# Kernel optimization log

Hardware: AMD Instinct MI355X
Metric: run time of the kernel (lower is better)

Reference implementation:

```python
import jax, jax.numpy as jnp
import numpy as np

B, T, C = 8, 2048, 1024


def setup_inputs() -> dict:
    key = jax.random.key(0)
    ks = jax.random.split(key, 7)
    s = 0.02  # typical init scale for weights
    return {
        "x": jax.random.normal(ks[0], (B, T, C), jnp.float32),
        "wq": jax.random.normal(ks[1], (C, C), jnp.float32) * s,
        "bq": jax.random.normal(ks[2], (C,), jnp.float32) * s,
        "wk": jax.random.normal(ks[3], (C, C), jnp.float32) * s,
        "bk": jax.random.normal(ks[4], (C,), jnp.float32) * s,
        "wv": jax.random.normal(ks[5], (C, C), jnp.float32) * s,
        "bv": jax.random.normal(ks[6], (C,), jnp.float32) * s,
    }


def reference(x, wq, bq, wk, bk, wv, bv):
    # x: [B, T, C]; torch Linear stores weight as [out, in] -> x @ W.T + b
    Bx, Tx, Cx = x.shape
    Q = x @ wq.T + bq  # [B, T, C]
    K = x @ wk.T + bk
    V = x @ wv.T + bv
    # NOTE: source computes K @ Q^T (keys index rows, queries index columns)
    scores = jnp.einsum("btc,bsc->bts", K, Q) / jnp.sqrt(jnp.float32(Cx))  # [B, T, T]
    causal = jnp.tril(jnp.ones((Tx, Tx), dtype=bool))  # mask==0 above diagonal
    scores = jnp.where(causal, scores, -jnp.inf)
    # torch masked_fill with a (1,1,T,T) mask broadcasts scores to (1,B,T,T)
    scores = scores[None]  # [1, B, T, T]
    w = jax.nn.softmax(scores, axis=-1)
    out = jnp.einsum("abts,bsc->abtc", w, V)  # [1, B, T, C]
    return out
```

## Files before the change

kernel.cpp:

```cpp
#include <hip/hip_runtime.h>
#include <stdint.h>

typedef unsigned short u16;
typedef __attribute__((ext_vector_type(8))) __bf16 bf16x8;
typedef __attribute__((ext_vector_type(4))) float f32x4;

#define DEVI __device__ __forceinline__

DEVI u16 f32_to_bf16(float f) {
  uint32_t u = __builtin_bit_cast(uint32_t, f);
  u += 0x7FFFu + ((u >> 16) & 1u);
  return (u16)(u >> 16);
}

DEVI void gl2lds16(const void* g, void* l) {
  __builtin_amdgcn_global_load_lds(
      (const __attribute__((address_space(1))) void*)g,
      (__attribute__((address_space(3))) void*)l, 16, 0, 0);
}

#define SMEM_U16 17408

#define S_BATCH 2228224

DEVI void gemm_bt_mainloop(const u16* __restrict__ A, const u16* __restrict__ B,
                           int lda, int ldb, int kIters,
                           u16* As, u16* Bs, f32x4 (&acc)[4][4]) {
  const int tid = threadIdx.x;
  const int lane = tid & 63;
  const int wid = tid >> 6;
  const int wr = wid >> 1, wc = wid & 1;
  const int l15 = lane & 15, quad = lane >> 4;

  const int srow = tid >> 3;
  const int sgrp = ((tid & 7) - srow) & 7;
  const u16* Ag = A + (size_t)srow * lda + sgrp * 8;
  const u16* Bg = B + (size_t)srow * ldb + sgrp * 8;
  char* AsDst = (char*)As + tid * 16;
  char* BsDst = (char*)Bs + tid * 16;

  const int a_row0 = wr * 64 + l15;
  const int b_row0 = wc * 64 + l15;

  for (int kb = 0; kb < kIters; ++kb) {
#pragma unroll
    for (int r = 0; r < 4; ++r) {
      gl2lds16(Ag + (size_t)(r * 32) * lda, AsDst + r * 4096);
      gl2lds16(Bg + (size_t)(r * 32) * ldb, BsDst + r * 4096);
    }
    Ag += 64;
    Bg += 64;
    __syncthreads();
#pragma unroll
    for (int kk = 0; kk < 2; ++kk) {
      const int gA = ((kk * 4 + quad + a_row0) & 7) * 8;
      const int gB = ((kk * 4 + quad + b_row0) & 7) * 8;
      bf16x8 af[4], bfr[4];
#pragma unroll
      for (int i = 0; i < 4; ++i)
        af[i] = *(const bf16x8*)(As + (a_row0 + i * 16) * 64 + gA);
#pragma unroll
      for (int j = 0; j < 4; ++j)
        bfr[j] = *(const bf16x8*)(Bs + (b_row0 + j * 16) * 64 + gB);
#pragma unroll
      for (int i = 0; i < 4; ++i)
#pragma unroll
        for (int j = 0; j < 4; ++j)
          acc[i][j] = __builtin_amdgcn_mfma_f32_16x16x32_bf16(af[i], bfr[j],
                                                              acc[i][j], 0, 0, 0);
    }
    __syncthreads();
  }
}

DEVI void store_tile_bf16(const u16* tile, u16* __restrict__ out, int ld_out) {
  const int tid = threadIdx.x;
  const int c0 = (tid & 15) * 8;
#pragma unroll
  for (int rr = 0; rr < 8; ++rr) {
    const int row = rr * 16 + (tid >> 4);
    const uint4 v = *(const uint4*)(tile + row * 136 + c0);
    *(uint4*)(out + (size_t)row * ld_out + c0) = v;
  }
}

__global__ void cast_f32_to_bf16_kernel(const float* __restrict__ src,
                                        u16* __restrict__ dst, int n4) {
  int i = blockIdx.x * blockDim.x + threadIdx.x;
  const int stride = gridDim.x * blockDim.x;
  for (; i < n4; i += stride) {
    const float4 v = ((const float4*)src)[i];
    ushort4 o;
    o.x = f32_to_bf16(v.x);
    o.y = f32_to_bf16(v.y);
    o.z = f32_to_bf16(v.z);
    o.w = f32_to_bf16(v.w);
    ((ushort4*)dst)[i] = o;
  }
}

__global__ void cast_w_kernel(const float* __restrict__ wq,
                              const float* __restrict__ wk,
                              const float* __restrict__ wv,
                              u16* __restrict__ wb, float* __restrict__ sums) {
  const int z = blockIdx.y;
  if (z == 3) {
    int i = blockIdx.x * blockDim.x + threadIdx.x;
    if (i < 4096) ((float4*)sums)[i] = (float4){0.f, 0.f, 0.f, 0.f};
    return;
  }
  const float* src = (z == 0) ? wq : (z == 1) ? wk : wv;
  u16* dst = wb + (size_t)z * 1048576;
  int i = blockIdx.x * blockDim.x + threadIdx.x;
  const int stride = gridDim.x * blockDim.x;
  for (; i < 262144; i += stride) {
    const float4 v = ((const float4*)src)[i];
    ushort4 o;
    o.x = f32_to_bf16(v.x);
    o.y = f32_to_bf16(v.y);
    o.z = f32_to_bf16(v.z);
    o.w = f32_to_bf16(v.w);
    ((ushort4*)dst)[i] = o;
  }
}

__global__ __launch_bounds__(256) void qkv_kernel(
    const u16* __restrict__ xb, const u16* __restrict__ wb,
    const float* __restrict__ bq, const float* __restrict__ bk,
    const float* __restrict__ bv, u16* __restrict__ Qb, u16* __restrict__ Kb,
    u16* __restrict__ Vt) {
  __shared__ __align__(16) u16 smem[SMEM_U16];
  u16* As = smem;
  u16* Bs = smem + 8192;

  const int id = blockIdx.x;
  const int xcd = id & 7;
  const int local = id >> 3;
  const int chunk = local >> 6;
  const int li = local & 63;
  const int x = (chunk % 3) * 8 + (li & 7);
  const int y = xcd * 16 + (chunk / 3) * 8 + (li >> 3);
  const int m0 = y * 128;
  const int z = x >> 3;
  const int n0 = (x & 7) * 128;
  const float* bias = (z == 0) ? bq : (z == 1) ? bk : bv;

  f32x4 acc[4][4];
#pragma unroll
  for (int i = 0; i < 4; ++i)
#pragma unroll
    for (int j = 0; j < 4; ++j) acc[i][j] = (f32x4){0.f, 0.f, 0.f, 0.f};

  const int tid = threadIdx.x;
  const int lane = tid & 63, wid = tid >> 6;
  const int wr = wid >> 1, wc = wid & 1;
  const int l15 = lane & 15, quad = lane >> 4;

  if (z < 2) {
    gemm_bt_mainloop(wb + (size_t)(x * 128) * 1024, xb + (size_t)m0 * 1024,
                     1024, 1024, 16, As, Bs, acc);
#pragma unroll
    for (int i = 0; i < 4; ++i) {
      const int c0 = wr * 64 + i * 16 + quad * 4;
      const float4 b4 = *(const float4*)(bias + n0 + c0);
#pragma unroll
      for (int j = 0; j < 4; ++j) {
        const int t = wc * 64 + j * 16 + l15;
        ushort4 o;
        o.x = f32_to_bf16(acc[i][j][0] + b4.x);
        o.y = f32_to_bf16(acc[i][j][1] + b4.y);
        o.z = f32_to_bf16(acc[i][j][2] + b4.z);
        o.w = f32_to_bf16(acc[i][j][3] + b4.w);
        *(ushort4*)(smem + t * 136 + c0) = o;
      }
    }
    __syncthreads();
    u16* Out = ((z == 0) ? Qb : Kb) + (size_t)m0 * 1024 + n0;
    store_tile_bf16(smem, Out, 1024);
  } else {
    gemm_bt_mainloop(xb + (size_t)m0 * 1024, wb + (size_t)(x * 128) * 1024,
                     1024, 1024, 16, As, Bs, acc);
#pragma unroll
    for (int j = 0; j < 4; ++j) {
      const int c = wc * 64 + j * 16 + l15;
      const float bb = bias[n0 + c];
#pragma unroll
      for (int i = 0; i < 4; ++i) {
        const int t = wr * 64 + i * 16 + quad * 4;
        ushort4 o;
        o.x = f32_to_bf16(acc[i][j][0] + bb);
        o.y = f32_to_bf16(acc[i][j][1] + bb);
        o.z = f32_to_bf16(acc[i][j][2] + bb);
        o.w = f32_to_bf16(acc[i][j][3] + bb);
        *(ushort4*)(smem + c * 136 + t) = o;
      }
    }
    __syncthreads();
    const int bidx = m0 >> 11;
    const int t0 = m0 & 2047;
    u16* Out = Vt + ((size_t)bidx * 1024 + n0) * 2048 + t0;
    store_tile_bf16(smem, Out, 2048);
  }
}

__global__ __launch_bounds__(256) void score_kernel(const u16* __restrict__ Kb,
                                                    const u16* __restrict__ Qb,
                                                    u16* __restrict__ Spk,
                                                    float* __restrict__ sums) {
  const int b = blockIdx.x & 7;
  const int l = 135 - (blockIdx.x >> 3);
  int rt = (int)((sqrtf(8.f * l + 1.f) - 1.f) * 0.5f);
  int ct = l - rt * (rt + 1) / 2;
  if (ct > rt) { ++rt; ct = l - rt * (rt + 1) / 2; }
  if (ct < 0)  { --rt; ct = l - rt * (rt + 1) / 2; }

  __shared__ __align__(16) u16 smem[SMEM_U16];
  u16* As = smem;
  u16* Bs = smem + 8192;

  f32x4 acc[4][4];
#pragma unroll
  for (int i = 0; i < 4; ++i)
#pragma unroll
    for (int j = 0; j < 4; ++j) acc[i][j] = (f32x4){0.f, 0.f, 0.f, 0.f};

  const u16* A = Qb + ((size_t)b * 2048 + ct * 128) * 1024;
  const u16* B = Kb + ((size_t)b * 2048 + rt * 128) * 1024;
  gemm_bt_mainloop(A, B, 1024, 1024, 16, As, Bs, acc);

  const int tid = threadIdx.x;
  const int lane = tid & 63, wid = tid >> 6;
  const int wr = wid >> 1, wc = wid & 1;
  const int l15 = lane & 15, quad = lane >> 4;
  const bool diag = (rt == ct);

  float sj[4] = {0.f, 0.f, 0.f, 0.f};
#pragma unroll
  for (int i = 0; i < 4; ++i) {
    const int s0 = wr * 64 + i * 16 + quad * 4;
#pragma unroll
    for (int j = 0; j < 4; ++j) {
      const int t = wc * 64 + j * 16 + l15;
      ushort4 o;
      float e[4];
#pragma unroll
      for (int r = 0; r < 4; ++r) {
        float v = __expf(acc[i][j][r] * 0.03125f);
        if (diag && (s0 + r) > t) v = 0.f;
        e[r] = v;
        sj[j] += v;
      }
      o.x = f32_to_bf16(e[0]);
      o.y = f32_to_bf16(e[1]);
      o.z = f32_to_bf16(e[2]);
      o.w = f32_to_bf16(e[3]);
      *(ushort4*)(smem + t * 136 + s0) = o;
    }
  }
#pragma unroll
  for (int j = 0; j < 4; ++j) {
    float v = sj[j];
    v += __shfl_xor(v, 16);
    v += __shfl_xor(v, 32);
    if (quad == 0)
      atomicAdd(&sums[(size_t)b * 2048 + rt * 128 + wc * 64 + j * 16 + l15], v);
  }
  __syncthreads();
  const int ld = (rt + 1) * 128;
  u16* Out = Spk + (size_t)b * S_BATCH + (size_t)(rt * (rt + 1) / 2) * 16384 +
             ct * 128;
  store_tile_bf16(smem, Out, ld);
}

__global__ __launch_bounds__(256) void pv_kernel(const u16* __restrict__ Spk,
                                                 const u16* __restrict__ Vt,
                                                 const float* __restrict__ sums,
                                                 float* __restrict__ Out) {
  const int b = blockIdx.x & 7;
  const int local = 127 - (blockIdx.x >> 3);
  const int rt = local >> 3;
  const int ct = local & 7;

  __shared__ __align__(16) u16 smem[SMEM_U16];
  u16* As = smem;
  u16* Bs = smem + 8192;
  float* ftile = (float*)smem;

  f32x4 acc[4][4];
#pragma unroll
  for (int i = 0; i < 4; ++i)
#pragma unroll
    for (int j = 0; j < 4; ++j) acc[i][j] = (f32x4){0.f, 0.f, 0.f, 0.f};

  const u16* A = Vt + ((size_t)b * 1024 + ct * 128) * 2048;
  const u16* B = Spk + (size_t)b * S_BATCH +
                 (size_t)(rt * (rt + 1) / 2) * 16384;
  const int ldb = (rt + 1) * 128;
  gemm_bt_mainloop(A, B, 2048, ldb, (rt + 1) * 2, As, Bs, acc);

  const int tid = threadIdx.x;
  const int lane = tid & 63, wid = tid >> 6;
  const int wr = wid >> 1, wc = wid & 1;
  const int l15 = lane & 15, quad = lane >> 4;

  const float* sumsb = sums + (size_t)b * 2048 + rt * 128;
  float* Ob = Out + (size_t)b * 2048 * 1024 + (size_t)(rt * 128) * 1024 +
              ct * 128;
#pragma unroll
  for (int h = 0; h < 2; ++h) {
    if (wc == h) {
#pragma unroll
      for (int j = 0; j < 4; ++j) {
        const int tl = j * 16 + l15;
        const float iv = 1.0f / sumsb[h * 64 + tl];
#pragma unroll
        for (int i = 0; i < 4; ++i) {
          const int c0 = wr * 64 + i * 16 + quad * 4;
          float4 v;
          v.x = acc[i][j][0] * iv;
          v.y = acc[i][j][1] * iv;
          v.z = acc[i][j][2] * iv;
          v.w = acc[i][j][3] * iv;
          *(float4*)(ftile + tl * 132 + c0) = v;
        }
      }
    }
    __syncthreads();
#pragma unroll
    for (int rr = 0; rr < 8; ++rr) {
      const int row = rr * 8 + (tid >> 5);
      const int c0 = (tid & 31) * 4;
      const float4 v = *(const float4*)(ftile + row * 132 + c0);
      *(float4*)(Ob + (size_t)(h * 64 + row) * 1024 + c0) = v;
    }
    __syncthreads();
  }
}

extern "C" void kernel_launch(void* const* d_in, const int* in_sizes, int n_in,
                              void* d_out, int out_size, void* d_ws,
                              size_t ws_size, hipStream_t stream) {
  const float* x = (const float*)d_in[0];
  const float* wq = (const float*)d_in[1];
  const float* bq = (const float*)d_in[2];
  const float* wk = (const float*)d_in[3];
  const float* bk = (const float*)d_in[4];
  const float* wv = (const float*)d_in[5];
  const float* bv = (const float*)d_in[6];
  float* out = (float*)d_out;
  char* ws = (char*)d_ws;

  u16* Qb = (u16*)(ws);
  u16* Kb = (u16*)(ws + ((size_t)32 << 20));
  u16* Vt = (u16*)(ws + ((size_t)64 << 20));
  u16* Spk = (u16*)(ws + ((size_t)96 << 20));
  u16* xb = (u16*)(ws + ((size_t)96 << 20));
  float* sums = (float*)(ws + ((size_t)132 << 20));
  u16* wb = (u16*)(ws + ((size_t)134 << 20));

  cast_f32_to_bf16_kernel<<<16384, 256, 0, stream>>>(x, xb, 16777216 / 4);
  cast_w_kernel<<<dim3(512, 4), 256, 0, stream>>>(wq, wk, wv, wb, sums);

  qkv_kernel<<<3072, 256, 0, stream>>>(xb, wb, bq, bk, bv, Qb, Kb, Vt);

  score_kernel<<<8 * 136, 256, 0, stream>>>(Kb, Qb, Spk, sums);

  pv_kernel<<<8 * 128, 256, 0, stream>>>(Spk, Vt, sums, out);
}
```

Measured before the change: 343.2 us.

## Rewrite QKV GEMM with 256x256 tiles and ping-pong LDS pipeline

Replaces the 128x128 QKV projection kernel, which used the shared mainloop, with a 512-thread, 256x256-tile kernel. It double-buffers 128KB of LDS filled by direct global-to-LDS loads with XOR swizzling, and interleaves quarter-tile MFMA phases with barriers, s_setprio and explicit waitcnt to overlap loads and compute. Larger tiles cut global traffic per FLOP and the block count drops from 3072 to 768. The cost is much higher LDS and register use, which limits occupancy, and fragile hand-scheduled synchronisation.

```diff
diff --git a/kernel.cpp b/kernel.cpp
--- a/kernel.cpp
+++ b/kernel.cpp
@@ -124,83 +124,230 @@
   }
 }
 
-__global__ __launch_bounds__(256) void qkv_kernel(
+__global__ __launch_bounds__(512, 2) void qkv_kernel(
     const u16* __restrict__ xb, const u16* __restrict__ wb,
     const float* __restrict__ bq, const float* __restrict__ bk,
     const float* __restrict__ bv, u16* __restrict__ Qb, u16* __restrict__ Kb,
     u16* __restrict__ Vt) {
-  __shared__ __align__(16) u16 smem[SMEM_U16];
-  u16* As = smem;
-  u16* Bs = smem + 8192;
+  __shared__ __align__(16) u16 lds[65536];
 
   const int id = blockIdx.x;
-  const int xcd = id & 7;
-  const int local = id >> 3;
-  const int chunk = local >> 6;
-  const int li = local & 63;
-  const int x = (chunk % 3) * 8 + (li & 7);
-  const int y = xcd * 16 + (chunk / 3) * 8 + (li >> 3);
-  const int m0 = y * 128;
-  const int z = x >> 3;
-  const int n0 = (x & 7) * 128;
-  const float* bias = (z == 0) ? bq : (z == 1) ? bk : bv;
-
-  f32x4 acc[4][4];
-#pragma unroll
-  for (int i = 0; i < 4; ++i)
-#pragma unroll
-    for (int j = 0; j < 4; ++j) acc[i][j] = (f32x4){0.f, 0.f, 0.f, 0.f};
+  const int wg = (id & 7) * 96 + (id >> 3);
+  const int g = wg >> 3, u = wg & 7;
+  const int z = g >> 5;
+  const int tp = g & 31;
+  const int tmt = tp * 2 + (u >> 2);
+  const int tct = u & 3;
+
+  int m0, n0;
+  const u16* Aptr;
+  const u16* Bptr;
+  if (z < 2) {
+    m0 = tct * 256;
+    n0 = tmt * 256;
+    Aptr = wb + (size_t)z * 1048576 + (size_t)m0 * 1024;
+    Bptr = xb + (size_t)n0 * 1024;
+  } else {
+    m0 = tmt * 256;
+    n0 = tct * 256;
+    Aptr = xb + (size_t)m0 * 1024;
+    Bptr = wb + (size_t)2 * 1048576 + (size_t)n0 * 1024;
+  }
 
   const int tid = threadIdx.x;
+  const int srow = tid >> 3;
+  const int sgrp = ((tid & 7) - srow) & 7;
+  const u16* Ag = Aptr + (size_t)srow * 1024 + sgrp * 8;
+  const u16* Bg = Bptr + (size_t)srow * 1024 + sgrp * 8;
+  char* ldsDst = (char*)lds + tid * 16;
+
+#define ST_A0(kt) do { const u16* s_ = Ag + (kt) * 64;           char* d_ = ldsDst + (((kt) & 1) * 65536);         gl2lds16(s_, d_); gl2lds16(s_ + 65536, d_ + 8192); } while (0)
+#define ST_A1(kt) do { const u16* s_ = Ag + 131072 + (kt) * 64;  char* d_ = ldsDst + (((kt) & 1) * 65536) + 16384; gl2lds16(s_, d_); gl2lds16(s_ + 65536, d_ + 8192); } while (0)
+#define ST_B0(kt) do { const u16* s_ = Bg + (kt) * 64;           char* d_ = ldsDst + (((kt) & 1) * 65536) + 32768; gl2lds16(s_, d_); gl2lds16(s_ + 65536, d_ + 8192); } while (0)
+#define ST_B1(kt) do { const u16* s_ = Bg + 131072 + (kt) * 64;  char* d_ = ldsDst + (((kt) & 1) * 65536) + 49152; gl2lds16(s_, d_); gl2lds16(s_ + 65536, d_ + 8192); } while (0)
+
+  ST_A0(0); ST_B0(0); ST_B1(0); ST_A1(0);
+  ST_A0(1); ST_B0(1); ST_B1(1);
+
   const int lane = tid & 63, wid = tid >> 6;
-  const int wr = wid >> 1, wc = wid & 1;
+  const int wr = wid >> 2, wc = wid & 3;
   const int l15 = lane & 15, quad = lane >> 4;
 
+  int aoff[4][2], boff[2][2];
+#pragma unroll
+  for (int i_ = 0; i_ < 4; ++i_) {
+    const int arow = wr * 64 + i_ * 16 + l15;
+#pragma unroll
+    for (int k_ = 0; k_ < 2; ++k_)
+      aoff[i_][k_] = arow * 64 + ((k_ * 4 + quad + arow) & 7) * 8;
+  }
+#pragma unroll
+  for (int j_ = 0; j_ < 2; ++j_) {
+    const int brow = wc * 32 + j_ * 16 + l15;
+#pragma unroll
+    for (int k_ = 0; k_ < 2; ++k_)
+      boff[j_][k_] = brow * 64 + ((k_ * 4 + quad + brow) & 7) * 8;
+  }
+
+  f32x4 acc[2][2][4][2];
+#pragma unroll
+  for (int a_ = 0; a_ < 2; ++a_)
+#pragma unroll
+    for (int b_ = 0; b_ < 2; ++b_)
+#pragma unroll
+      for (int i_ = 0; i_ < 4; ++i_)
+#pragma unroll
+        for (int j_ = 0; j_ < 2; ++j_)
+          acc[a_][b_][i_][j_] = (f32x4){0.f, 0.f, 0.f, 0.f};
+
+  bf16x8 af[4][2], bfr[2][2][2];
+
+#define LOADA(qm, buf) do { const u16* p_ = lds + (buf) * 32768 + (qm) * 8192; \
+  _Pragma("unroll") for (int i_ = 0; i_ < 4; ++i_) \
+  _Pragma("unroll") for (int k_ = 0; k_ < 2; ++k_) \
+    af[i_][k_] = *(const bf16x8*)(p_ + aoff[i_][k_]); } while (0)
+#define LOADB(qn, buf) do { const u16* p_ = lds + (buf) * 32768 + 16384 + (qn) * 8192; \
+  _Pragma("unroll") for (int j_ = 0; j_ < 2; ++j_) \
+  _Pragma("unroll") for (int k_ = 0; k_ < 2; ++k_) \
+    bfr[qn][j_][k_] = *(const bf16x8*)(p_ + boff[j_][k_]); } while (0)
+#define MMA(qm, qn) do { \
+  _Pragma("unroll") for (int i_ = 0; i_ < 4; ++i_) \
+  _Pragma("unroll") for (int j_ = 0; j_ < 2; ++j_) \
+  _Pragma("unroll") for (int k_ = 0; k_ < 2; ++k_) \
+    acc[qm][qn][i_][j_] = __builtin_amdgcn_mfma_f32_16x16x32_bf16( \
+        af[i_][k_], bfr[qn][j_][k_], acc[qm][qn][i_][j_], 0, 0, 0); } while (0)
+
+#define BAR __builtin_amdgcn_s_barrier()
+#define WLG0 asm volatile("s_waitcnt lgkmcnt(0)")
+#define WLG8 asm volatile("s_waitcnt lgkmcnt(8)")
+#define PRIO1 __builtin_amdgcn_s_setprio(1)
+#define PRIO0 __builtin_amdgcn_s_setprio(0)
+
+  asm volatile("s_waitcnt vmcnt(6)" ::: "memory");
+  BAR;
+
+#pragma unroll 1
+  for (int it = 0; it < 7; ++it) {
+    const int j0 = 2 * it;
+    LOADA(0, 0); LOADB(0, 0); ST_A1(j0 + 1); WLG8;
+    BAR; WLG0; PRIO1; MMA(0, 0); PRIO0; BAR;
+    LOADB(1, 0); ST_A0(j0 + 2);
+    BAR; WLG0; PRIO1; MMA(0, 1); PRIO0; BAR;
+    LOADA(1, 0); ST_B0(j0 + 2);
+    BAR; WLG0; PRIO1; MMA(1, 1); PRIO0; BAR;
+    ST_B1(j0 + 2);
+    BAR; PRIO1; MMA(1, 0); PRIO0;
+    asm volatile("s_waitcnt vmcnt(6)" ::: "memory");
+    BAR;
+    LOADA(0, 1); LOADB(0, 1); ST_A1(j0 + 2); WLG8;
+    BAR; WLG0; PRIO1; MMA(0, 0); PRIO0; BAR;
+    LOADB(1, 1); ST_A0(j0 + 3);
+    BAR; WLG0; PRIO1; MMA(0, 1); PRIO0; BAR;
+    LOADA(1, 1); ST_B0(j0 + 3);
+    BAR; WLG0; PRIO1; MMA(1, 1); PRIO0; BAR;
+    ST_B1(j0 + 3);
+    BAR; PRIO1; MMA(1, 0); PRIO0;
+    asm volatile("s_waitcnt vmcnt(6)" ::: "memory");
+    BAR;
+  }
+  {
+    LOADA(0, 0); LOADB(0, 0); ST_A1(15); WLG8;
+    BAR; WLG0; PRIO1; MMA(0, 0); PRIO0; BAR;
+    LOADB(1, 0);
+    BAR; WLG0; PRIO1; MMA(0, 1); PRIO0; BAR;
+    LOADA(1, 0);
+    BAR; WLG0; PRIO1; MMA(1, 1); PRIO0; BAR;
+    PRIO1; MMA(1, 0); PRIO0;
+    asm volatile("s_waitcnt vmcnt(0)" ::: "memory");
+    BAR;
+    LOADA(0, 1); LOADB(0, 1); WLG8;
+    BAR; WLG0; PRIO1; MMA(0, 0); PRIO0; BAR;
+    LOADB(1, 1);
+    BAR; WLG0; PRIO1; MMA(0, 1); PRIO0; BAR;
+    LOADA(1, 1);
+    BAR; WLG0; PRIO1; MMA(1, 1); PRIO0; BAR;
+    PRIO1; MMA(1, 0); PRIO0;
+    BAR;
+  }
+
   if (z < 2) {
-    gemm_bt_mainloop(wb + (size_t)(x * 128) * 1024, xb + (size_t)m0 * 1024,
-                     1024, 1024, 16, As, Bs, acc);
-#pragma unroll
-    for (int i = 0; i < 4; ++i) {
-      const int c0 = wr * 64 + i * 16 + quad * 4;
-      const float4 b4 = *(const float4*)(bias + n0 + c0);
-#pragma unroll
-      for (int j = 0; j < 4; ++j) {
-        const int t = wc * 64 + j * 16 + l15;
-        ushort4 o;
-        o.x = f32_to_bf16(acc[i][j][0] + b4.x);
-        o.y = f32_to_bf16(acc[i][j][1] + b4.y);
-        o.z = f32_to_bf16(acc[i][j][2] + b4.z);
-        o.w = f32_to_bf16(acc[i][j][3] + b4.w);
-        *(ushort4*)(smem + t * 136 + c0) = o;
+    const float* bias = (z == 0) ? bq : bk;
+    u16* Out = (z == 0) ? Qb : Kb;
+#pragma unroll
+    for (int th = 0; th < 2; ++th) {
+      if (th) __syncthreads();
+#pragma unroll
+      for (int qm = 0; qm < 2; ++qm)
+#pragma unroll
+        for (int i_ = 0; i_ < 4; ++i_) {
+          const int c = qm * 128 + wr * 64 + i_ * 16 + quad * 4;
+          const float4 b4 = *(const float4*)(bias + m0 + c);
+#pragma unroll
+          for (int j_ = 0; j_ < 2; ++j_) {
+            const int row = wc * 32 + j_ * 16 + l15;
+            ushort4 o;
+            o.x = f32_to_bf16(acc[qm][th][i_][j_][0] + b4.x);
+            o.y = f32_to_bf16(acc[qm][th][i_][j_][1] + b4.y);
+            o.z = f32_to_bf16(acc[qm][th][i_][j_][2] + b4.z);
+            o.w = f32_to_bf16(acc[qm][th][i_][j_][3] + b4.w);
+            *(ushort4*)(lds + row * 264 + c) = o;
+          }
+        }
+      __syncthreads();
+#pragma unroll
+      for (int p = 0; p < 8; ++p) {
+        const int row = p * 16 + (tid >> 5);
+        const int c0 = (tid & 31) * 8;
+        const uint4 v = *(const uint4*)(lds + row * 264 + c0);
+        *(uint4*)(Out + (size_t)(n0 + th * 128 + row) * 1024 + m0 + c0) = v;
       }
     }
-    __syncthreads();
-    u16* Out = ((z == 0) ? Qb : Kb) + (size_t)m0 * 1024 + n0;
-    store_tile_bf16(smem, Out, 1024);
   } else {
-    gemm_bt_mainloop(xb + (size_t)m0 * 1024, wb + (size_t)(x * 128) * 1024,
-                     1024, 1024, 16, As, Bs, acc);
-#pragma unroll
-    for (int j = 0; j < 4; ++j) {
-      const int c = wc * 64 + j * 16 + l15;
-      const float bb = bias[n0 + c];
-#pragma unroll
-      for (int i = 0; i < 4; ++i) {
-        const int t = wr * 64 + i * 16 + quad * 4;
-        ushort4 o;
-        o.x = f32_to_bf16(acc[i][j][0] + bb);
-        o.y = f32_to_bf16(acc[i][j][1] + bb);
-        o.z = f32_to_bf16(acc[i][j][2] + bb);
-        o.w = f32_to_bf16(acc[i][j][3] + bb);
-        *(ushort4*)(smem + c * 136 + t) = o;
+    const int b = m0 >> 11;
+    const int t0b = m0 & 2047;
+    u16* Out = Vt + (size_t)b * 2097152;
+#pragma unroll
+    for (int th = 0; th < 2; ++th) {
+      if (th) __syncthreads();
+#pragma unroll
+      for (int j_ = 0; j_ < 2; ++j_) {
+        const int row = wc * 32 + j_ * 16 + l15;
+        const float bb = bv[n0 + th * 128 + row];
+#pragma unroll
+        for (int qm = 0; qm < 2; ++qm)
+#pragma unroll
+          for (int i_ = 0; i_ < 4; ++i_) {
+            const int c = qm * 128 + wr * 64 + i_ * 16 + quad * 4;
+            ushort4 o;
+            o.x = f32_to_bf16(acc[qm][th][i_][j_][0] + bb);
+            o.y = f32_to_bf16(acc[qm][th][i_][j_][1] + bb);
+            o.z = f32_to_bf16(acc[qm][th][i_][j_][2] + bb);
+            o.w = f32_to_bf16(acc[qm][th][i_][j_][3] + bb);
+            *(ushort4*)(lds + row * 264 + c) = o;
+          }
       }
-    }
-    __syncthreads();
-    const int bidx = m0 >> 11;
-    const int t0 = m0 & 2047;
-    u16* Out = Vt + ((size_t)bidx * 1024 + n0) * 2048 + t0;
-    store_tile_bf16(smem, Out, 2048);
-  }
+      __syncthreads();
+#pragma unroll
+      for (int p = 0; p < 8; ++p) {
+        const int row = p * 16 + (tid >> 5);
+        const int c0 = (tid & 31) * 8;
+        const uint4 v = *(const uint4*)(lds + row * 264 + c0);
+        *(uint4*)(Out + (size_t)(n0 + th * 128 + row) * 2048 + t0b + c0) = v;
+      }
+    }
+  }
+#undef ST_A0
+#undef ST_A1
+#undef ST_B0
+#undef ST_B1
+#undef LOADA
+#undef LOADB
+#undef MMA
+#undef BAR
+#undef WLG0
+#undef WLG8
+#undef PRIO1
+#undef PRIO0
 }
 
 __global__ __launch_bounds__(256) void score_kernel(const u16* __restrict__ Kb,
@@ -361,7 +508,7 @@
   cast_f32_to_bf16_kernel<<<16384, 256, 0, stream>>>(x, xb, 16777216 / 4);
   cast_w_kernel<<<dim3(512, 4), 256, 0, stream>>>(wq, wk, wv, wb, sums);
 
-  qkv_kernel<<<3072, 256, 0, stream>>>(xb, wb, bq, bk, bv, Qb, Kb, Vt);
+  qkv_kernel<<<768, 512, 0, stream>>>(xb, wb, bq, bk, bv, Qb, Kb, Vt);
 
   score_kernel<<<8 * 136, 256, 0, stream>>>(Kb, Qb, Spk, sums);
 
```

After: 337.7 us. No clear change (-1.6%).
